# Kernel optimization log

Hardware: AMD Instinct MI355X
Metric: run time of the kernel (lower is better)

## Reference

```python
import jax, jax.numpy as jnp
import numpy as np

DIM = 1024
NUM_HEADS = 16
HEAD_DIM = DIM // NUM_HEADS
EPS = 1e-5


def setup_inputs() -> dict:
    key = jax.random.key(0)
    ks = jax.random.split(key, 8)
    B, N = 4, 2048
    s = 0.02
    return {
        "x1": jax.random.normal(ks[0], (B, N, DIM), jnp.float32),
        "x2": jax.random.normal(ks[1], (B, N, DIM), jnp.float32),
        "wq": jax.random.normal(ks[2], (DIM, DIM), jnp.float32) * s,
        "bq": jnp.zeros((DIM,), jnp.float32),
        "wkv": jax.random.normal(ks[3], (DIM, 2 * DIM), jnp.float32) * s,
        "bkv": jnp.zeros((2 * DIM,), jnp.float32),
        "gamma_q": jnp.ones((HEAD_DIM,), jnp.float32),
        "beta_q": jnp.zeros((HEAD_DIM,), jnp.float32),
        "gamma_k": jnp.ones((HEAD_DIM,), jnp.float32),
        "beta_k": jnp.zeros((HEAD_DIM,), jnp.float32),
    }


def _layernorm(x, gamma, beta):
    m = jnp.mean(x, axis=-1, keepdims=True)
    v = jnp.mean(jnp.square(x - m), axis=-1, keepdims=True)
    return (x - m) * jax.lax.rsqrt(v + EPS) * gamma + beta


def reference(x1, x2, wq, bq, wkv, bkv, gamma_q, beta_q, gamma_k, beta_k):
    B, N, C = x1.shape
    H, D = NUM_HEADS, C // NUM_HEADS
    q = x1 @ wq + bq                      # [B,N,C]
    kv = x2 @ wkv + bkv                   # [B,N,2C]
    k, v = kv[..., :C], kv[..., C:]
    # [B,N,C] -> [B,H,N,D]
    q = q.reshape(B, N, H, D).transpose(0, 2, 1, 3)
    k = k.reshape(B, N, H, D).transpose(0, 2, 1, 3)
    v = v.reshape(B, N, H, D).transpose(0, 2, 1, 3)
    q = _layernorm(q, gamma_q, beta_q)
    k = _layernorm(k, gamma_k, beta_k)
    scale = 1.0 / jnp.sqrt(jnp.asarray(D, x1.dtype))
    scores = jnp.einsum("bhnd,bhmd->bhnm", q, k) * scale
    attn = jax.nn.softmax(scores, axis=-1)
    out = jnp.einsum("bhnm,bhmd->bhnd", attn, v)  # [B,H,N,D]
    return out.transpose(0, 2, 1, 3).reshape(B, N, C)
```

## Files before the change

### kernel.cpp

```cpp
#include <hip/hip_runtime.h>
#include <hip/hip_bf16.h>

#define NHEADS 16
#define HDIM 64
#define BATCH 4
#define SEQ 2048
#define CDIM 1024
#define ROWS (BATCH * SEQ)
#define QSCALE (0.125f * 1.44269504088896f)

typedef __attribute__((ext_vector_type(8))) short short8;
typedef __attribute__((ext_vector_type(4))) float f32x4;
typedef __attribute__((ext_vector_type(4))) unsigned int u32x4;
typedef __attribute__((ext_vector_type(2))) unsigned int u32x2;

__device__ inline short f2bf(float f) {
    unsigned int u = __builtin_bit_cast(unsigned int, f);
    unsigned int r = (u + 0x7fffu + ((u >> 16) & 1u)) >> 16;
    return (short)r;
}

__device__ __forceinline__ void gll16(const void* g, void* l) {
    __builtin_amdgcn_global_load_lds(
        (const __attribute__((address_space(1))) unsigned int*)g,
        (__attribute__((address_space(3))) unsigned int*)l, 16, 0, 0);
}

__device__ __forceinline__ unsigned int pack_bf2(float a, float b) {
    return __builtin_amdgcn_perm(__builtin_bit_cast(unsigned int, b),
                                 __builtin_bit_cast(unsigned int, a), 0x07060302u);
}

__global__ __launch_bounds__(256) void cvt_bf16(const float* __restrict__ src,
                                                short* __restrict__ dst, int n8) {
    int i = blockIdx.x * 256 + threadIdx.x;
    if (i < n8) {
        f32x4 a = ((const f32x4*)src)[i * 2];
        f32x4 b = ((const f32x4*)src)[i * 2 + 1];
        short8 o;
        o[0] = f2bf(a[0]); o[1] = f2bf(a[1]); o[2] = f2bf(a[2]); o[3] = f2bf(a[3]);
        o[4] = f2bf(b[0]); o[5] = f2bf(b[1]); o[6] = f2bf(b[2]); o[7] = f2bf(b[3]);
        ((short8*)dst)[i] = o;
    }
}

__global__ __launch_bounds__(256) void wtrans(const float* __restrict__ W,
                                              short* __restrict__ WT, int Nw) {
    __shared__ short T[64][72];
    const int t = threadIdx.x;
    const int n0 = blockIdx.x * 64, k0 = blockIdx.y * 64;
    const int kl = t >> 2, c4 = (t & 3) * 16;
    const float* src = W + (size_t)(k0 + kl) * Nw + n0 + c4;
    short8 s0, s1;
#pragma unroll
    for (int e = 0; e < 2; e++) {
        f32x4 u = *(const f32x4*)(src + e * 4);
        s0[e * 4 + 0] = f2bf(u[0]); s0[e * 4 + 1] = f2bf(u[1]);
        s0[e * 4 + 2] = f2bf(u[2]); s0[e * 4 + 3] = f2bf(u[3]);
        f32x4 v = *(const f32x4*)(src + 8 + e * 4);
        s1[e * 4 + 0] = f2bf(v[0]); s1[e * 4 + 1] = f2bf(v[1]);
        s1[e * 4 + 2] = f2bf(v[2]); s1[e * 4 + 3] = f2bf(v[3]);
    }
    *(short8*)&T[kl][c4] = s0;
    *(short8*)&T[kl][c4 + 8] = s1;
    __syncthreads();
#pragma unroll
    for (int pass = 0; pass < 2; pass++) {
        int n = (t >> 3) + pass * 32;
        short8 o;
#pragma unroll
        for (int e = 0; e < 8; e++) o[e] = T[(t & 7) * 8 + e][n];
        *(short8*)(WT + (size_t)(n0 + n) * 1024 + k0 + (t & 7) * 8) = o;
    }
}

__global__ __launch_bounds__(256) void gemm_q_ln(
    const short* __restrict__ A,
    const short* __restrict__ BT,
    const float* __restrict__ bias,
    const float* __restrict__ gamma,
    const float* __restrict__ beta,
    short* __restrict__ Out)
{
    __shared__ short As[128][32];
    __shared__ short Bs[128][32];

    const int tid = threadIdx.x;
    const int wave = tid >> 6, lane = tid & 63;
    const int wr = wave >> 1, wc = wave & 1;
    const int quad = lane >> 4, l15 = lane & 15;
    const int rblk = blockIdx.y, cblk = blockIdx.x;

    f32x4 acc[4][4];
#pragma unroll
    for (int i = 0; i < 4; i++)
#pragma unroll
        for (int j = 0; j < 4; j++) acc[i][j] = f32x4{0.f, 0.f, 0.f, 0.f};

    const int srow = wave * 32 + (lane >> 2);
    const int scol = (lane & 3) * 8;

    for (int k0 = 0; k0 < CDIM; k0 += 32) {
        __syncthreads();
#pragma unroll
        for (int c = 0; c < 2; c++) {
            gll16(A + (size_t)(rblk * 128 + srow + c * 16) * CDIM + k0 + scol,
                  &As[srow + c * 16][scol]);
            gll16(BT + (size_t)(cblk * 128 + srow + c * 16) * CDIM + k0 + scol,
                  &Bs[srow + c * 16][scol]);
        }
        __syncthreads();

        short8 af[4], bfr[4];
#pragma unroll
        for (int i = 0; i < 4; i++)
            af[i] = *(const short8*)&As[wr * 64 + i * 16 + l15][quad * 8];
#pragma unroll
        for (int j = 0; j < 4; j++)
            bfr[j] = *(const short8*)&Bs[wc * 64 + j * 16 + l15][quad * 8];
#pragma unroll
        for (int i = 0; i < 4; i++)
#pragma unroll
            for (int j = 0; j < 4; j++)
                acc[i][j] = __builtin_amdgcn_mfma_f32_16x16x32_bf16(af[i], bfr[j], acc[i][j], 0, 0, 0);
    }

    const int col0 = cblk * 128 + wc * 64;
    const int h = col0 >> 6;
    float bv[4], gv[4], btv[4];
#pragma unroll
    for (int j = 0; j < 4; j++) {
        int d = j * 16 + l15;
        bv[j] = bias[col0 + d];
        gv[j] = gamma[d];
        btv[j] = beta[d];
    }
#pragma unroll
    for (int i = 0; i < 4; i++) {
        int rowl = rblk * 128 + wr * 64 + i * 16 + quad * 4;
#pragma unroll
        for (int reg = 0; reg < 4; reg++) {
            float x[4], s = 0.f, s2 = 0.f;
#pragma unroll
            for (int j = 0; j < 4; j++) {
                x[j] = acc[i][j][reg] + bv[j];
                s += x[j];
                s2 += x[j] * x[j];
            }
#pragma unroll
            for (int m = 1; m < 16; m <<= 1) {
                s += __shfl_xor(s, m);
                s2 += __shfl_xor(s2, m);
            }
            float mean = s * (1.f / 64.f);
            float var = s2 * (1.f / 64.f) - mean * mean;
            float rstd = rsqrtf(var + 1e-5f);
            int r = rowl + reg;
            int b = r >> 11, n = r & (SEQ - 1);
            size_t base = (((size_t)b * NHEADS + h) * SEQ + n) * 64;
#pragma unroll
            for (int j = 0; j < 4; j++) {
                float y = ((x[j] - mean) * rstd * gv[j] + btv[j]) * QSCALE;
                Out[base + j * 16 + l15] = f2bf(y);
            }
        }
    }
}

__global__ __launch_bounds__(256) void gemm_kv(
    const short* __restrict__ A,
    const short* __restrict__ BT,
    const float* __restrict__ bias,
    const float* __restrict__ gamma,
    const float* __restrict__ beta,
    short* __restrict__ KOut,
    short* __restrict__ VT)
{
    __shared__ short As[128][32];
    __shared__ short Bs[128][32];
    __shared__ short Ts[4][64][68];

    const int tid = threadIdx.x;
    const int wave = tid >> 6, lane = tid & 63;
    const int wr = wave >> 1, wc = wave & 1;
    const int quad = lane >> 4, l15 = lane & 15;
    const int rblk = blockIdx.y, cblk = blockIdx.x;

    f32x4 acc[4][4];
#pragma unroll
    for (int i = 0; i < 4; i++)
#pragma unroll
        for (int j = 0; j < 4; j++) acc[i][j] = f32x4{0.f, 0.f, 0.f, 0.f};

    const int srow = wave * 32 + (lane >> 2);
    const int scol = (lane & 3) * 8;

    for (int k0 = 0; k0 < CDIM; k0 += 32) {
        __syncthreads();
#pragma unroll
        for (int c = 0; c < 2; c++) {
            gll16(A + (size_t)(rblk * 128 + srow + c * 16) * CDIM + k0 + scol,
                  &As[srow + c * 16][scol]);
            gll16(BT + (size_t)(cblk * 128 + srow + c * 16) * CDIM + k0 + scol,
                  &Bs[srow + c * 16][scol]);
        }
        __syncthreads();

        short8 af[4], bfr[4];
#pragma unroll
        for (int i = 0; i < 4; i++)
            af[i] = *(const short8*)&As[wr * 64 + i * 16 + l15][quad * 8];
#pragma unroll
        for (int j = 0; j < 4; j++)
            bfr[j] = *(const short8*)&Bs[wc * 64 + j * 16 + l15][quad * 8];
#pragma unroll
        for (int i = 0; i < 4; i++)
#pragma unroll
            for (int j = 0; j < 4; j++)
                acc[i][j] = __builtin_amdgcn_mfma_f32_16x16x32_bf16(af[i], bfr[j], acc[i][j], 0, 0, 0);
    }

    const int col0 = cblk * 128 + wc * 64;
    const int g = col0 >> 6;
    float bv[4];
#pragma unroll
    for (int j = 0; j < 4; j++) bv[j] = bias[col0 + j * 16 + l15];

    if (g < NHEADS) {
        const int h = g;
        float gv[4], btv[4];
#pragma unroll
        for (int j = 0; j < 4; j++) {
            int d = j * 16 + l15;
            gv[j] = gamma[d];
            btv[j] = beta[d];
        }
#pragma unroll
        for (int i = 0; i < 4; i++) {
            int rowl = rblk * 128 + wr * 64 + i * 16 + quad * 4;
#pragma unroll
            for (int reg = 0; reg < 4; reg++) {
                float x[4], s = 0.f, s2 = 0.f;
#pragma unroll
                for (int j = 0; j < 4; j++) {
                    x[j] = acc[i][j][reg] + bv[j];
                    s += x[j];
                    s2 += x[j] * x[j];
                }
#pragma unroll
                for (int m = 1; m < 16; m <<= 1) {
                    s += __shfl_xor(s, m);
                    s2 += __shfl_xor(s2, m);
                }
                float mean = s * (1.f / 64.f);
                float var = s2 * (1.f / 64.f) - mean * mean;
                float rstd = rsqrtf(var + 1e-5f);
                int r = rowl + reg;
                int b = r >> 11, n = r & (SEQ - 1);
                size_t base = (((size_t)b * NHEADS + h) * SEQ + n) * 64;
#pragma unroll
                for (int j = 0; j < 4; j++) {
                    float y = (x[j] - mean) * rstd * gv[j] + btv[j];
                    KOut[base + j * 16 + l15] = f2bf(y);
                }
            }
        }
    } else {
        const int h = g - NHEADS;
#pragma unroll
        for (int i = 0; i < 4; i++)
#pragma unroll
            for (int reg = 0; reg < 4; reg++)
#pragma unroll
                for (int j = 0; j < 4; j++)
                    Ts[wave][i * 16 + quad * 4 + reg][j * 16 + l15] =
                        f2bf(acc[i][j][reg] + bv[j]);
        const int r = rblk * 128 + wr * 64 + lane;
        const int b = r >> 11, n = r & (SEQ - 1);
        const size_t vtbase = (((size_t)b * NHEADS + h) * 64) * SEQ;
#pragma unroll
        for (int e8 = 0; e8 < 8; e8++) {
            short8 v = *(const short8*)&Ts[wave][lane][e8 * 8];
#pragma unroll
            for (int e = 0; e < 8; e++)
                VT[vtbase + (size_t)(e8 * 8 + e) * SEQ + n] = v[e];
        }
    }
}

template <int JD, bool FIRST>
__device__ __forceinline__ void band_store(float* __restrict__ Ot,
                                           const f32x4 (&o)[4][4],
                                           int l15, int q) {
#pragma unroll
    for (int qc = 0; qc < 4; qc++)
#pragma unroll
        for (int reg = 0; reg < 4; reg++) {
            float* dst = &Ot[(qc * 16 + l15) * 68 + JD * 16 + q * 4 + reg];
            if (FIRST) *dst = o[JD][qc][reg];
            else       *dst += o[JD][qc][reg];
        }
}

__global__ __launch_bounds__(256, 2) void attn_fa(
    const short* __restrict__ Q,
    const short* __restrict__ Kk,
    const short* __restrict__ VT,
    float* __restrict__ Out)
{
    __shared__ __align__(16) char smem_raw[20480];

    const int tid = threadIdx.x;
    const int w = tid >> 6, lane = tid & 63;
    const int q = lane >> 4, l15 = lane & 15;
    const int bh = blockIdx.x;
    const int b = bh >> 4, h = bh & 15;
    const int qt = blockIdx.y;
    const size_t hb = (size_t)bh * SEQ * 64;
    const size_t vb = (size_t)bh * 64 * SEQ;

    unsigned int* Pd = (unsigned int*)smem_raw + w * 1280;
    float* Ot = (float*)smem_raw;
    float* Lred = (float*)smem_raw + 64 * 68;

    short8 qf[4][2];
#pragma unroll
    for (int qc = 0; qc < 4; qc++)
#pragma unroll
        for (int dh = 0; dh < 2; dh++)
            qf[qc][dh] = *(const short8*)(Q + hb +
                (size_t)(qt * 64 + qc * 16 + l15) * 64 + dh * 32 + q * 8);

    short8 ones;
#pragma unroll
    for (int e = 0; e < 8; e++) ones[e] = (short)0x3F80;

    f32x4 o[4][4];
#pragma unroll
    for (int jd = 0; jd < 4; jd++)
#pragma unroll
        for (int qc = 0; qc < 4; qc++) o[jd][qc] = f32x4{0.f, 0.f, 0.f, 0.f};
    f32x4 osum[4];
#pragma unroll
    for (int qc = 0; qc < 4; qc++) osum[qc] = f32x4{0.f, 0.f, 0.f, 0.f};

    const short* kbase = Kk + hb + (size_t)(w * 32 + l15) * 64 + q * 8;
    const short* vbase = VT + vb + (size_t)l15 * SEQ + w * 32 + q * 8;

    for (int kti = 0; kti < 16; kti++) {
        short8 kf[2][2];
#pragma unroll
        for (int kt = 0; kt < 2; kt++)
#pragma unroll
            for (int dh = 0; dh < 2; dh++)
                kf[kt][dh] = *(const short8*)(kbase +
                    (size_t)(kti * 128 + kt * 16) * 64 + dh * 32);
        short8 vf[4];
#pragma unroll
        for (int jd = 0; jd < 4; jd++)
            vf[jd] = *(const short8*)(vbase + (size_t)(jd * 16) * SEQ + kti * 128);

#pragma unroll
        for (int kt = 0; kt < 2; kt++)
#pragma unroll
            for (int qc = 0; qc < 4; qc++) {
                f32x4 z = f32x4{0.f, 0.f, 0.f, 0.f};
                z = __builtin_amdgcn_mfma_f32_16x16x32_bf16(kf[kt][0], qf[qc][0], z, 0, 0, 0);
                z = __builtin_amdgcn_mfma_f32_16x16x32_bf16(kf[kt][1], qf[qc][1], z, 0, 0, 0);
                u32x2 d2;
                d2[0] = pack_bf2(__builtin_amdgcn_exp2f(z[0]), __builtin_amdgcn_exp2f(z[1]));
                d2[1] = pack_bf2(__builtin_amdgcn_exp2f(z[2]), __builtin_amdgcn_exp2f(z[3]));
                *(u32x2*)&Pd[(qc * 16 + l15) * 20 + kt * 8 + 2 * q] = d2;
            }

        short8 pf[4];
#pragma unroll
        for (int qc = 0; qc < 4; qc++) {
            u32x4 pr = *(const u32x4*)&Pd[(qc * 16 + l15) * 20 + 4 * q];
            pf[qc] = __builtin_bit_cast(short8, pr);
        }

#pragma unroll
        for (int qc = 0; qc < 4; qc++)
            osum[qc] = __builtin_amdgcn_mfma_f32_16x16x32_bf16(ones, pf[qc], osum[qc], 0, 0, 0);
#pragma unroll
        for (int jd = 0; jd < 4; jd++)
#pragma unroll
            for (int qc = 0; qc < 4; qc++)
                o[jd][qc] = __builtin_amdgcn_mfma_f32_16x16x32_bf16(vf[jd], pf[qc], o[jd][qc], 0, 0, 0);
    }

    __syncthreads();
#pragma unroll
    for (int p = 0; p < 4; p++) {
        const int jd = (w + p) & 3;
        if (p == 0) {
            switch (jd) {
            case 0: band_store<0, true>(Ot, o, l15, q); break;
            case 1: band_store<1, true>(Ot, o, l15, q); break;
            case 2: band_store<2, true>(Ot, o, l15, q); break;
            case 3: band_store<3, true>(Ot, o, l15, q); break;
            }
            if (q == 0) {
#pragma unroll
                for (int qc = 0; qc < 4; qc++)
                    Lred[w * 64 + qc * 16 + l15] = osum[qc][0];
            }
        } else {
            switch (jd) {
            case 0: band_store<0, false>(Ot, o, l15, q); break;
            case 1: band_store<1, false>(Ot, o, l15, q); break;
            case 2: band_store<2, false>(Ot, o, l15, q); break;
            case 3: band_store<3, false>(Ot, o, l15, q); break;
            }
        }
        __syncthreads();
    }

    const int row = tid >> 2, c = tid & 3;
    float l = Lred[row] + Lred[64 + row] + Lred[128 + row] + Lred[192 + row];
    float inv = 1.f / l;
    float* obase = Out + ((size_t)b * SEQ + qt * 64 + row) * CDIM + h * 64;
#pragma unroll
    for (int i = 0; i < 4; i++) {
        f32x4 t = *(const f32x4*)&Ot[row * 68 + (c + 4 * i) * 4];
        *(f32x4*)(obase + (c + 4 * i) * 4) = t * inv;
    }
}

extern "C" void kernel_launch(void* const* d_in, const int* in_sizes, int n_in,
                              void* d_out, int out_size, void* d_ws, size_t ws_size,
                              hipStream_t stream) {
    const float* x1 = (const float*)d_in[0];
    const float* x2 = (const float*)d_in[1];
    const float* wq = (const float*)d_in[2];
    const float* bq = (const float*)d_in[3];
    const float* wkv = (const float*)d_in[4];
    const float* bkv = (const float*)d_in[5];
    const float* gq = (const float*)d_in[6];
    const float* btq = (const float*)d_in[7];
    const float* gk = (const float*)d_in[8];
    const float* btk = (const float*)d_in[9];
    float* out = (float*)d_out;

    short* a1 = (short*)d_ws;
    short* a2 = a1 + (size_t)ROWS * CDIM;
    short* wqT = a2 + (size_t)ROWS * CDIM;
    short* wkvT = wqT + (size_t)CDIM * CDIM;
    short* qln = wkvT + (size_t)2 * CDIM * CDIM;
    short* kln = qln + (size_t)ROWS * CDIM;
    short* vt = kln + (size_t)ROWS * CDIM;

    const int n8 = ROWS * CDIM / 8;
    cvt_bf16<<<dim3(n8 / 256), 256, 0, stream>>>(x1, a1, n8);
    cvt_bf16<<<dim3(n8 / 256), 256, 0, stream>>>(x2, a2, n8);
    wtrans<<<dim3(16, 16), 256, 0, stream>>>(wq, wqT, CDIM);
    wtrans<<<dim3(32, 16), 256, 0, stream>>>(wkv, wkvT, 2 * CDIM);

    gemm_q_ln<<<dim3(8, 64), 256, 0, stream>>>(a1, wqT, bq, gq, btq, qln);
    gemm_kv<<<dim3(16, 64), 256, 0, stream>>>(a2, wkvT, bkv, gk, btk, kln, vt);
    attn_fa<<<dim3(64, 32), 256, 0, stream>>>(qln, kln, vt, out);
}
```

Baseline: 349.0 us.

## Merge Q and KV projection GEMMs into one launch with swizzled block order

Replaces the separate Q-projection and KV-projection GEMM kernels with one kernel over a 24x64 grid. Each block chooses its input, weights and epilogue (Q layernorm with scale, K layernorm, or V transpose) from its column index. Block indices are swizzled so that groups of blocks share row tiles, aiming for better L2 reuse. The V-transpose staging buffer now reuses the shared-memory tile region, which lowers LDS use but needs an extra barrier. This removes one launch and the tail between the two GEMMs, at the cost of some per-block branching.

```diff
diff --git a/kernel.cpp b/kernel.cpp
--- a/kernel.cpp
+++ b/kernel.cpp
@@ -74,22 +74,37 @@
     }
 }
 
-__global__ __launch_bounds__(256) void gemm_q_ln(
-    const short* __restrict__ A,
-    const short* __restrict__ BT,
-    const float* __restrict__ bias,
-    const float* __restrict__ gamma,
-    const float* __restrict__ beta,
-    short* __restrict__ Out)
+__global__ __launch_bounds__(256) void gemm_fused(
+    const short* __restrict__ A1,
+    const short* __restrict__ A2,
+    const short* __restrict__ WQT,
+    const short* __restrict__ WKVT,
+    const float* __restrict__ bq,
+    const float* __restrict__ bkv,
+    const float* __restrict__ gq, const float* __restrict__ btq,
+    const float* __restrict__ gk, const float* __restrict__ btk,
+    short* __restrict__ QOut,
+    short* __restrict__ KOut,
+    short* __restrict__ VT)
 {
-    __shared__ short As[128][32];
-    __shared__ short Bs[128][32];
+    __shared__ __align__(16) char smem[34816];
+    short (*As)[32] = (short (*)[32])smem;
+    short (*Bs)[32] = (short (*)[32])(smem + 8192);
 
     const int tid = threadIdx.x;
     const int wave = tid >> 6, lane = tid & 63;
     const int wr = wave >> 1, wc = wave & 1;
     const int quad = lane >> 4, l15 = lane & 15;
-    const int rblk = blockIdx.y, cblk = blockIdx.x;
+
+    const int lin = blockIdx.y * 24 + blockIdx.x;
+    const int swz = (lin & 7) * 192 + (lin >> 3);
+    const int rblk = swz / 24;
+    const int cblkg = swz - rblk * 24;
+
+    const bool isQ = cblkg < 8;
+    const int cblk = isQ ? cblkg : cblkg - 8;
+    const short* Ap = isQ ? A1 : A2;
+    const short* BT = isQ ? WQT : WKVT;
 
     f32x4 acc[4][4];
 #pragma unroll
@@ -104,7 +119,7 @@
         __syncthreads();
 #pragma unroll
         for (int c = 0; c < 2; c++) {
-            gll16(A + (size_t)(rblk * 128 + srow + c * 16) * CDIM + k0 + scol,
+            gll16(Ap + (size_t)(rblk * 128 + srow + c * 16) * CDIM + k0 + scol,
                   &As[srow + c * 16][scol]);
             gll16(BT + (size_t)(cblk * 128 + srow + c * 16) * CDIM + k0 + scol,
                   &Bs[srow + c * 16][scol]);
@@ -126,112 +141,20 @@
     }
 
     const int col0 = cblk * 128 + wc * 64;
-    const int h = col0 >> 6;
-    float bv[4], gv[4], btv[4];
-#pragma unroll
-    for (int j = 0; j < 4; j++) {
-        int d = j * 16 + l15;
-        bv[j] = bias[col0 + d];
-        gv[j] = gamma[d];
-        btv[j] = beta[d];
-    }
-#pragma unroll
-    for (int i = 0; i < 4; i++) {
-        int rowl = rblk * 128 + wr * 64 + i * 16 + quad * 4;
-#pragma unroll
-        for (int reg = 0; reg < 4; reg++) {
-            float x[4], s = 0.f, s2 = 0.f;
-#pragma unroll
-            for (int j = 0; j < 4; j++) {
-                x[j] = acc[i][j][reg] + bv[j];
-                s += x[j];
-                s2 += x[j] * x[j];
-            }
-#pragma unroll
-            for (int m = 1; m < 16; m <<= 1) {
-                s += __shfl_xor(s, m);
-                s2 += __shfl_xor(s2, m);
-            }
-            float mean = s * (1.f / 64.f);
-            float var = s2 * (1.f / 64.f) - mean * mean;
-            float rstd = rsqrtf(var + 1e-5f);
-            int r = rowl + reg;
-            int b = r >> 11, n = r & (SEQ - 1);
-            size_t base = (((size_t)b * NHEADS + h) * SEQ + n) * 64;
-#pragma unroll
-            for (int j = 0; j < 4; j++) {
-                float y = ((x[j] - mean) * rstd * gv[j] + btv[j]) * QSCALE;
-                Out[base + j * 16 + l15] = f2bf(y);
-            }
-        }
-    }
-}
-
-__global__ __launch_bounds__(256) void gemm_kv(
-    const short* __restrict__ A,
-    const short* __restrict__ BT,
-    const float* __restrict__ bias,
-    const float* __restrict__ gamma,
-    const float* __restrict__ beta,
-    short* __restrict__ KOut,
-    short* __restrict__ VT)
-{
-    __shared__ short As[128][32];
-    __shared__ short Bs[128][32];
-    __shared__ short Ts[4][64][68];
-
-    const int tid = threadIdx.x;
-    const int wave = tid >> 6, lane = tid & 63;
-    const int wr = wave >> 1, wc = wave & 1;
-    const int quad = lane >> 4, l15 = lane & 15;
-    const int rblk = blockIdx.y, cblk = blockIdx.x;
-
-    f32x4 acc[4][4];
-#pragma unroll
-    for (int i = 0; i < 4; i++)
-#pragma unroll
-        for (int j = 0; j < 4; j++) acc[i][j] = f32x4{0.f, 0.f, 0.f, 0.f};
-
-    const int srow = wave * 32 + (lane >> 2);
-    const int scol = (lane & 3) * 8;
-
-    for (int k0 = 0; k0 < CDIM; k0 += 32) {
-        __syncthreads();
-#pragma unroll
-        for (int c = 0; c < 2; c++) {
-            gll16(A + (size_t)(rblk * 128 + srow + c * 16) * CDIM + k0 + scol,
-                  &As[srow + c * 16][scol]);
-            gll16(BT + (size_t)(cblk * 128 + srow + c * 16) * CDIM + k0 + scol,
-                  &Bs[srow + c * 16][scol]);
-        }
-        __syncthreads();
-
-        short8 af[4], bfr[4];
-#pragma unroll
-        for (int i = 0; i < 4; i++)
-            af[i] = *(const short8*)&As[wr * 64 + i * 16 + l15][quad * 8];
-#pragma unroll
-        for (int j = 0; j < 4; j++)
-            bfr[j] = *(const short8*)&Bs[wc * 64 + j * 16 + l15][quad * 8];
-#pragma unroll
-        for (int i = 0; i < 4; i++)
-#pragma unroll
-            for (int j = 0; j < 4; j++)
-                acc[i][j] = __builtin_amdgcn_mfma_f32_16x16x32_bf16(af[i], bfr[j], acc[i][j], 0, 0, 0);
-    }
-
-    const int col0 = cblk * 128 + wc * 64;
     const int g = col0 >> 6;
-    float bv[4];
-#pragma unroll
-    for (int j = 0; j < 4; j++) bv[j] = bias[col0 + j * 16 + l15];
-
-    if (g < NHEADS) {
+
+    if (cblkg < 16) {
+        const float* bias  = isQ ? bq : bkv;
+        const float* gamma = isQ ? gq : gk;
+        const float* beta  = isQ ? btq : btk;
+        short* Out = isQ ? QOut : KOut;
+        const float scale = isQ ? QSCALE : 1.f;
         const int h = g;
-        float gv[4], btv[4];
+        float bv[4], gv[4], btv[4];
 #pragma unroll
         for (int j = 0; j < 4; j++) {
             int d = j * 16 + l15;
+            bv[j] = bias[col0 + d];
             gv[j] = gamma[d];
             btv[j] = beta[d];
         }
@@ -260,13 +183,15 @@
                 size_t base = (((size_t)b * NHEADS + h) * SEQ + n) * 64;
 #pragma unroll
                 for (int j = 0; j < 4; j++) {
-                    float y = (x[j] - mean) * rstd * gv[j] + btv[j];
-                    KOut[base + j * 16 + l15] = f2bf(y);
+                    float y = ((x[j] - mean) * rstd * gv[j] + btv[j]) * scale;
+                    Out[base + j * 16 + l15] = f2bf(y);
                 }
             }
         }
     } else {
         const int h = g - NHEADS;
+        __syncthreads();
+        short (*Ts)[64][68] = (short (*)[64][68])smem;
 #pragma unroll
         for (int i = 0; i < 4; i++)
 #pragma unroll
@@ -274,7 +199,7 @@
 #pragma unroll
                 for (int j = 0; j < 4; j++)
                     Ts[wave][i * 16 + quad * 4 + reg][j * 16 + l15] =
-                        f2bf(acc[i][j][reg] + bv[j]);
+                        f2bf(acc[i][j][reg] + bkv[col0 + j * 16 + l15]);
         const int r = rblk * 128 + wr * 64 + lane;
         const int b = r >> 11, n = r & (SEQ - 1);
         const size_t vtbase = (((size_t)b * NHEADS + h) * 64) * SEQ;
@@ -457,7 +382,7 @@
     wtrans<<<dim3(16, 16), 256, 0, stream>>>(wq, wqT, CDIM);
     wtrans<<<dim3(32, 16), 256, 0, stream>>>(wkv, wkvT, 2 * CDIM);
 
-    gemm_q_ln<<<dim3(8, 64), 256, 0, stream>>>(a1, wqT, bq, gq, btq, qln);
-    gemm_kv<<<dim3(16, 64), 256, 0, stream>>>(a2, wkvT, bkv, gk, btk, kln, vt);
+    gemm_fused<<<dim3(24, 64), 256, 0, stream>>>(a1, a2, wqT, wkvT, bq, bkv,
+                                                 gq, btq, gk, btk, qln, kln, vt);
     attn_fa<<<dim3(64, 32), 256, 0, stream>>>(qln, kln, vt, out);
 }
```

New measurement: 371.0 us. 1.06x slower.

## Deepen GEMM K-tile to 64, alias LDS for transpose, swizzle block order

Applied to the files above, without the earlier changes.

Both projection GEMMs now stage 64-wide K slices in LDS instead of 32. That halves the number of barrier pairs per K loop and issues more global-to-LDS loads per sync. The kv kernel reuses the A/B staging buffer for the V transpose scratch, adding a barrier, so total LDS stays about the same. All three kernels remap the linear block index with an XCD-style swizzle, which is meant to keep blocks sharing operand tiles on the same chiplet for better L2 locality. The attention remap assumes a specific grid shape.

```diff
diff --git a/kernel.cpp b/kernel.cpp
--- a/kernel.cpp
+++ b/kernel.cpp
@@ -82,14 +82,16 @@
     const float* __restrict__ beta,
     short* __restrict__ Out)
 {
-    __shared__ short As[128][32];
-    __shared__ short Bs[128][32];
+    __shared__ short As[128][64];
+    __shared__ short Bs[128][64];
 
     const int tid = threadIdx.x;
     const int wave = tid >> 6, lane = tid & 63;
     const int wr = wave >> 1, wc = wave & 1;
     const int quad = lane >> 4, l15 = lane & 15;
-    const int rblk = blockIdx.y, cblk = blockIdx.x;
+    const int lin = blockIdx.y * 8 + blockIdx.x;
+    const int swz = (lin & 7) * 64 + (lin >> 3);
+    const int rblk = swz >> 3, cblk = swz & 7;
 
     f32x4 acc[4][4];
 #pragma unroll
@@ -97,32 +99,35 @@
 #pragma unroll
         for (int j = 0; j < 4; j++) acc[i][j] = f32x4{0.f, 0.f, 0.f, 0.f};
 
-    const int srow = wave * 32 + (lane >> 2);
-    const int scol = (lane & 3) * 8;
-
-    for (int k0 = 0; k0 < CDIM; k0 += 32) {
-        __syncthreads();
-#pragma unroll
-        for (int c = 0; c < 2; c++) {
-            gll16(A + (size_t)(rblk * 128 + srow + c * 16) * CDIM + k0 + scol,
-                  &As[srow + c * 16][scol]);
-            gll16(BT + (size_t)(cblk * 128 + srow + c * 16) * CDIM + k0 + scol,
-                  &Bs[srow + c * 16][scol]);
-        }
-        __syncthreads();
-
-        short8 af[4], bfr[4];
-#pragma unroll
-        for (int i = 0; i < 4; i++)
-            af[i] = *(const short8*)&As[wr * 64 + i * 16 + l15][quad * 8];
-#pragma unroll
-        for (int j = 0; j < 4; j++)
-            bfr[j] = *(const short8*)&Bs[wc * 64 + j * 16 + l15][quad * 8];
-#pragma unroll
-        for (int i = 0; i < 4; i++)
+    const int srow = wave * 8 + (lane >> 3);
+    const int scol = (lane & 7) * 8;
+
+    for (int k0 = 0; k0 < CDIM; k0 += 64) {
+        __syncthreads();
+#pragma unroll
+        for (int c = 0; c < 4; c++) {
+            gll16(A + (size_t)(rblk * 128 + srow + c * 32) * CDIM + k0 + scol,
+                  &As[srow + c * 32][scol]);
+            gll16(BT + (size_t)(cblk * 128 + srow + c * 32) * CDIM + k0 + scol,
+                  &Bs[srow + c * 32][scol]);
+        }
+        __syncthreads();
+
+#pragma unroll
+        for (int kk = 0; kk < 2; kk++) {
+            short8 af[4], bfr[4];
+#pragma unroll
+            for (int i = 0; i < 4; i++)
+                af[i] = *(const short8*)&As[wr * 64 + i * 16 + l15][kk * 32 + quad * 8];
 #pragma unroll
             for (int j = 0; j < 4; j++)
-                acc[i][j] = __builtin_amdgcn_mfma_f32_16x16x32_bf16(af[i], bfr[j], acc[i][j], 0, 0, 0);
+                bfr[j] = *(const short8*)&Bs[wc * 64 + j * 16 + l15][kk * 32 + quad * 8];
+#pragma unroll
+            for (int i = 0; i < 4; i++)
+#pragma unroll
+                for (int j = 0; j < 4; j++)
+                    acc[i][j] = __builtin_amdgcn_mfma_f32_16x16x32_bf16(af[i], bfr[j], acc[i][j], 0, 0, 0);
+        }
     }
 
     const int col0 = cblk * 128 + wc * 64;
@@ -176,15 +181,17 @@
     short* __restrict__ KOut,
     short* __restrict__ VT)
 {
-    __shared__ short As[128][32];
-    __shared__ short Bs[128][32];
-    __shared__ short Ts[4][64][68];
+    __shared__ __align__(16) char smem[34816];
+    short (*As)[64] = (short (*)[64])smem;
+    short (*Bs)[64] = (short (*)[64])(smem + 16384);
 
     const int tid = threadIdx.x;
     const int wave = tid >> 6, lane = tid & 63;
     const int wr = wave >> 1, wc = wave & 1;
     const int quad = lane >> 4, l15 = lane & 15;
-    const int rblk = blockIdx.y, cblk = blockIdx.x;
+    const int lin = blockIdx.y * 16 + blockIdx.x;
+    const int swz = (lin & 7) * 128 + (lin >> 3);
+    const int rblk = swz >> 4, cblk = swz & 15;
 
     f32x4 acc[4][4];
 #pragma unroll
@@ -192,32 +199,35 @@
 #pragma unroll
         for (int j = 0; j < 4; j++) acc[i][j] = f32x4{0.f, 0.f, 0.f, 0.f};
 
-    const int srow = wave * 32 + (lane >> 2);
-    const int scol = (lane & 3) * 8;
-
-    for (int k0 = 0; k0 < CDIM; k0 += 32) {
-        __syncthreads();
-#pragma unroll
-        for (int c = 0; c < 2; c++) {
-            gll16(A + (size_t)(rblk * 128 + srow + c * 16) * CDIM + k0 + scol,
-                  &As[srow + c * 16][scol]);
-            gll16(BT + (size_t)(cblk * 128 + srow + c * 16) * CDIM + k0 + scol,
-                  &Bs[srow + c * 16][scol]);
-        }
-        __syncthreads();
-
-        short8 af[4], bfr[4];
-#pragma unroll
-        for (int i = 0; i < 4; i++)
-            af[i] = *(const short8*)&As[wr * 64 + i * 16 + l15][quad * 8];
-#pragma unroll
-        for (int j = 0; j < 4; j++)
-            bfr[j] = *(const short8*)&Bs[wc * 64 + j * 16 + l15][quad * 8];
-#pragma unroll
-        for (int i = 0; i < 4; i++)
+    const int srow = wave * 8 + (lane >> 3);
+    const int scol = (lane & 7) * 8;
+
+    for (int k0 = 0; k0 < CDIM; k0 += 64) {
+        __syncthreads();
+#pragma unroll
+        for (int c = 0; c < 4; c++) {
+            gll16(A + (size_t)(rblk * 128 + srow + c * 32) * CDIM + k0 + scol,
+                  &As[srow + c * 32][scol]);
+            gll16(BT + (size_t)(cblk * 128 + srow + c * 32) * CDIM + k0 + scol,
+                  &Bs[srow + c * 32][scol]);
+        }
+        __syncthreads();
+
+#pragma unroll
+        for (int kk = 0; kk < 2; kk++) {
+            short8 af[4], bfr[4];
+#pragma unroll
+            for (int i = 0; i < 4; i++)
+                af[i] = *(const short8*)&As[wr * 64 + i * 16 + l15][kk * 32 + quad * 8];
 #pragma unroll
             for (int j = 0; j < 4; j++)
-                acc[i][j] = __builtin_amdgcn_mfma_f32_16x16x32_bf16(af[i], bfr[j], acc[i][j], 0, 0, 0);
+                bfr[j] = *(const short8*)&Bs[wc * 64 + j * 16 + l15][kk * 32 + quad * 8];
+#pragma unroll
+            for (int i = 0; i < 4; i++)
+#pragma unroll
+                for (int j = 0; j < 4; j++)
+                    acc[i][j] = __builtin_amdgcn_mfma_f32_16x16x32_bf16(af[i], bfr[j], acc[i][j], 0, 0, 0);
+        }
     }
 
     const int col0 = cblk * 128 + wc * 64;
@@ -267,6 +277,8 @@
         }
     } else {
         const int h = g - NHEADS;
+        __syncthreads();
+        short (*Ts)[64][68] = (short (*)[64][68])smem;
 #pragma unroll
         for (int i = 0; i < 4; i++)
 #pragma unroll
@@ -313,9 +325,11 @@
     const int tid = threadIdx.x;
     const int w = tid >> 6, lane = tid & 63;
     const int q = lane >> 4, l15 = lane & 15;
-    const int bh = blockIdx.x;
+    const int lin = blockIdx.y * 64 + blockIdx.x;
+    const int swz = (lin & 7) * 256 + (lin >> 3);
+    const int bh = swz >> 5;
+    const int qt = swz & 31;
     const int b = bh >> 4, h = bh & 15;
-    const int qt = blockIdx.y;
     const size_t hb = (size_t)bh * SEQ * 64;
     const size_t vb = (size_t)bh * 64 * SEQ;
 
```

New measurement: 353.5 us. About the same (+1.3%).

## Software-pipeline attention loop with double-buffered P and prefetched K/V; swizzle block order

Applied to the files above, without the earlier changes.

Restructures the attention inner loop into a two-stage software pipeline. Each step computes the QK^T exponentials for the next tile into one of two LDS P buffers while the PV MFMAs consume the previous buffer, and it prefetches the following K/V fragments into alternating registers. This is meant to hide global load latency and the LDS round-trip behind MFMA work. All three kernels also remap block indices with a modulo-8 swizzle to change which tiles run together, probably for cache locality or XCD spreading. In exchange, LDS use doubles to 40KB and register pressure rises, which may reduce occupancy.

```diff
diff --git a/kernel.cpp b/kernel.cpp
--- a/kernel.cpp
+++ b/kernel.cpp
@@ -89,7 +89,9 @@
     const int wave = tid >> 6, lane = tid & 63;
     const int wr = wave >> 1, wc = wave & 1;
     const int quad = lane >> 4, l15 = lane & 15;
-    const int rblk = blockIdx.y, cblk = blockIdx.x;
+    const int lin = blockIdx.y * 8 + blockIdx.x;
+    const int swz = (lin & 7) * 64 + (lin >> 3);
+    const int rblk = swz >> 3, cblk = swz & 7;
 
     f32x4 acc[4][4];
 #pragma unroll
@@ -184,7 +186,9 @@
     const int wave = tid >> 6, lane = tid & 63;
     const int wr = wave >> 1, wc = wave & 1;
     const int quad = lane >> 4, l15 = lane & 15;
-    const int rblk = blockIdx.y, cblk = blockIdx.x;
+    const int lin = blockIdx.y * 16 + blockIdx.x;
+    const int swz = (lin & 7) * 128 + (lin >> 3);
+    const int rblk = swz >> 4, cblk = swz & 15;
 
     f32x4 acc[4][4];
 #pragma unroll
@@ -302,24 +306,80 @@
         }
 }
 
+__device__ __forceinline__ void attn_body(
+    int t, bool doLoad,
+    const short* __restrict__ kbase, const short* __restrict__ vbase,
+    const short8 (&qf)[4][2], const short8& ones,
+    short8 (&kfCur)[2][2], short8 (&kfNxt)[2][2], short8 (&vfPN)[4],
+    unsigned int* __restrict__ PdW, unsigned int* __restrict__ PdR,
+    int l15, int q, f32x4 (&o)[4][4], f32x4 (&osum)[4])
+{
+    short8 pf[4];
+#pragma unroll
+    for (int qc = 0; qc < 4; qc++) {
+        u32x4 pr = *(const u32x4*)&PdR[(qc * 16 + l15) * 20 + 4 * q];
+        pf[qc] = __builtin_bit_cast(short8, pr);
+    }
+
+#pragma unroll
+    for (int kt = 0; kt < 2; kt++)
+#pragma unroll
+        for (int qc = 0; qc < 4; qc++) {
+            f32x4 z = f32x4{0.f, 0.f, 0.f, 0.f};
+            z = __builtin_amdgcn_mfma_f32_16x16x32_bf16(kfCur[kt][0], qf[qc][0], z, 0, 0, 0);
+            z = __builtin_amdgcn_mfma_f32_16x16x32_bf16(kfCur[kt][1], qf[qc][1], z, 0, 0, 0);
+            u32x2 d2;
+            d2[0] = pack_bf2(__builtin_amdgcn_exp2f(z[0]), __builtin_amdgcn_exp2f(z[1]));
+            d2[1] = pack_bf2(__builtin_amdgcn_exp2f(z[2]), __builtin_amdgcn_exp2f(z[3]));
+            *(u32x2*)&PdW[(qc * 16 + l15) * 20 + kt * 8 + 2 * q] = d2;
+        }
+
+    if (doLoad) {
+#pragma unroll
+        for (int kt = 0; kt < 2; kt++)
+#pragma unroll
+            for (int dh = 0; dh < 2; dh++)
+                kfNxt[kt][dh] = *(const short8*)(kbase +
+                    (size_t)((t + 1) * 128 + kt * 16) * 64 + dh * 32);
+    }
+
+#pragma unroll
+    for (int qc = 0; qc < 4; qc++)
+        osum[qc] = __builtin_amdgcn_mfma_f32_16x16x32_bf16(ones, pf[qc], osum[qc], 0, 0, 0);
+#pragma unroll
+    for (int jd = 0; jd < 4; jd++)
+#pragma unroll
+        for (int qc = 0; qc < 4; qc++)
+            o[jd][qc] = __builtin_amdgcn_mfma_f32_16x16x32_bf16(vfPN[jd], pf[qc], o[jd][qc], 0, 0, 0);
+
+    if (doLoad) {
+#pragma unroll
+        for (int jd = 0; jd < 4; jd++)
+            vfPN[jd] = *(const short8*)(vbase + (size_t)(jd * 16) * SEQ + (t + 1) * 128);
+    }
+}
+
 __global__ __launch_bounds__(256, 2) void attn_fa(
     const short* __restrict__ Q,
     const short* __restrict__ Kk,
     const short* __restrict__ VT,
     float* __restrict__ Out)
 {
-    __shared__ __align__(16) char smem_raw[20480];
+    __shared__ __align__(16) char smem_raw[40960];
 
     const int tid = threadIdx.x;
     const int w = tid >> 6, lane = tid & 63;
     const int q = lane >> 4, l15 = lane & 15;
-    const int bh = blockIdx.x;
+    const int lin = blockIdx.y * 64 + blockIdx.x;
+    const int swz = (lin & 7) * 256 + (lin >> 3);
+    const int bh = swz >> 5;
+    const int qt = swz & 31;
     const int b = bh >> 4, h = bh & 15;
-    const int qt = blockIdx.y;
     const size_t hb = (size_t)bh * SEQ * 64;
     const size_t vb = (size_t)bh * 64 * SEQ;
 
-    unsigned int* Pd = (unsigned int*)smem_raw + w * 1280;
+    unsigned int* PdA = (unsigned int*)smem_raw + w * 2560;
+    unsigned int* PdB = PdA + 1280;
     float* Ot = (float*)smem_raw;
     float* Lred = (float*)smem_raw + 64 * 68;
 
@@ -347,39 +407,50 @@
     const short* kbase = Kk + hb + (size_t)(w * 32 + l15) * 64 + q * 8;
     const short* vbase = VT + vb + (size_t)l15 * SEQ + w * 32 + q * 8;
 
-    for (int kti = 0; kti < 16; kti++) {
-        short8 kf[2][2];
-#pragma unroll
-        for (int kt = 0; kt < 2; kt++)
-#pragma unroll
-            for (int dh = 0; dh < 2; dh++)
-                kf[kt][dh] = *(const short8*)(kbase +
-                    (size_t)(kti * 128 + kt * 16) * 64 + dh * 32);
-        short8 vf[4];
-#pragma unroll
-        for (int jd = 0; jd < 4; jd++)
-            vf[jd] = *(const short8*)(vbase + (size_t)(jd * 16) * SEQ + kti * 128);
-
-#pragma unroll
-        for (int kt = 0; kt < 2; kt++)
-#pragma unroll
-            for (int qc = 0; qc < 4; qc++) {
-                f32x4 z = f32x4{0.f, 0.f, 0.f, 0.f};
-                z = __builtin_amdgcn_mfma_f32_16x16x32_bf16(kf[kt][0], qf[qc][0], z, 0, 0, 0);
-                z = __builtin_amdgcn_mfma_f32_16x16x32_bf16(kf[kt][1], qf[qc][1], z, 0, 0, 0);
-                u32x2 d2;
-                d2[0] = pack_bf2(__builtin_amdgcn_exp2f(z[0]), __builtin_amdgcn_exp2f(z[1]));
-                d2[1] = pack_bf2(__builtin_amdgcn_exp2f(z[2]), __builtin_amdgcn_exp2f(z[3]));
-                *(u32x2*)&Pd[(qc * 16 + l15) * 20 + kt * 8 + 2 * q] = d2;
-            }
-
+    short8 kfA[2][2], kfB[2][2], vfA[4], vfB[4];
+
+#pragma unroll
+    for (int kt = 0; kt < 2; kt++)
+#pragma unroll
+        for (int dh = 0; dh < 2; dh++)
+            kfA[kt][dh] = *(const short8*)(kbase + (size_t)(kt * 16) * 64 + dh * 32);
+#pragma unroll
+    for (int jd = 0; jd < 4; jd++)
+        vfA[jd] = *(const short8*)(vbase + (size_t)(jd * 16) * SEQ);
+#pragma unroll
+    for (int kt = 0; kt < 2; kt++)
+#pragma unroll
+        for (int qc = 0; qc < 4; qc++) {
+            f32x4 z = f32x4{0.f, 0.f, 0.f, 0.f};
+            z = __builtin_amdgcn_mfma_f32_16x16x32_bf16(kfA[kt][0], qf[qc][0], z, 0, 0, 0);
+            z = __builtin_amdgcn_mfma_f32_16x16x32_bf16(kfA[kt][1], qf[qc][1], z, 0, 0, 0);
+            u32x2 d2;
+            d2[0] = pack_bf2(__builtin_amdgcn_exp2f(z[0]), __builtin_amdgcn_exp2f(z[1]));
+            d2[1] = pack_bf2(__builtin_amdgcn_exp2f(z[2]), __builtin_amdgcn_exp2f(z[3]));
+            *(u32x2*)&PdA[(qc * 16 + l15) * 20 + kt * 8 + 2 * q] = d2;
+        }
+#pragma unroll
+    for (int kt = 0; kt < 2; kt++)
+#pragma unroll
+        for (int dh = 0; dh < 2; dh++)
+            kfB[kt][dh] = *(const short8*)(kbase + (size_t)(128 + kt * 16) * 64 + dh * 32);
+#pragma unroll
+    for (int jd = 0; jd < 4; jd++)
+        vfB[jd] = *(const short8*)(vbase + (size_t)(jd * 16) * SEQ + 128);
+
+    for (int t = 1; t < 15; t += 2) {
+        attn_body(t,     true, kbase, vbase, qf, ones, kfB, kfA, vfA, PdB, PdA, l15, q, o, osum);
+        attn_body(t + 1, true, kbase, vbase, qf, ones, kfA, kfB, vfB, PdA, PdB, l15, q, o, osum);
+    }
+    attn_body(15, false, kbase, vbase, qf, ones, kfB, kfA, vfA, PdB, PdA, l15, q, o, osum);
+
+    {
         short8 pf[4];
 #pragma unroll
         for (int qc = 0; qc < 4; qc++) {
-            u32x4 pr = *(const u32x4*)&Pd[(qc * 16 + l15) * 20 + 4 * q];
+            u32x4 pr = *(const u32x4*)&PdB[(qc * 16 + l15) * 20 + 4 * q];
             pf[qc] = __builtin_bit_cast(short8, pr);
         }
-
 #pragma unroll
         for (int qc = 0; qc < 4; qc++)
             osum[qc] = __builtin_amdgcn_mfma_f32_16x16x32_bf16(ones, pf[qc], osum[qc], 0, 0, 0);
@@ -387,7 +458,7 @@
         for (int jd = 0; jd < 4; jd++)
 #pragma unroll
             for (int qc = 0; qc < 4; qc++)
-                o[jd][qc] = __builtin_amdgcn_mfma_f32_16x16x32_bf16(vf[jd], pf[qc], o[jd][qc], 0, 0, 0);
+                o[jd][qc] = __builtin_amdgcn_mfma_f32_16x16x32_bf16(vfB[jd], pf[qc], o[jd][qc], 0, 0, 0);
     }
 
     __syncthreads();
```

After: 338.6 us. 3.0% less time.
